# Kernel tuning notes

Hardware: AMD Instinct MI355X
Metric: run time of the kernel (lower is better)

Reference implementation:

```python
import jax, jax.numpy as jnp
import numpy as np

N_NODES = 50000
N_EDGES = 800000
IN_CH = 64
OUT_CH = 128
N_HEADS = 4
HEAD_DIM = OUT_CH // N_HEADS
LN_EPS = 1e-5


def setup_inputs() -> dict:
    key = jax.random.key(0)
    ks = jax.random.split(key, 12)
    def lin(k, fan_in, fan_out):
        bound = 1.0 / np.sqrt(fan_in)
        kw, kb = jax.random.split(k)
        W = jax.random.uniform(kw, (fan_in, fan_out), jnp.float32, -bound, bound)
        b = jax.random.uniform(kb, (fan_out,), jnp.float32, -bound, bound)
        return W, b
    Wq, bq = lin(ks[0], IN_CH, OUT_CH)
    Wk, bk = lin(ks[1], IN_CH, OUT_CH)
    Wv, bv = lin(ks[2], IN_CH, OUT_CH)
    We1, be1 = lin(ks[3], 2 * IN_CH, OUT_CH)
    We2, be2 = lin(ks[4], OUT_CH, N_HEADS)
    Wo, bo = lin(ks[5], OUT_CH, OUT_CH)
    gamma = jnp.ones((OUT_CH,), jnp.float32)
    beta = jnp.zeros((OUT_CH,), jnp.float32)
    x = jax.random.normal(ks[6], (N_NODES, IN_CH), jnp.float32)
    edge_index = jax.random.randint(ks[7], (2, N_EDGES), 0, N_NODES, jnp.int64 if jax.config.jax_enable_x64 else jnp.int32)
    return {"x": x, "edge_index": edge_index,
            "Wq": Wq, "bq": bq, "Wk": Wk, "bk": bk, "Wv": Wv, "bv": bv,
            "We1": We1, "be1": be1, "We2": We2, "be2": be2,
            "Wo": Wo, "bo": bo, "gamma": gamma, "beta": beta}


def reference(x, edge_index, Wq, bq, Wk, bk, Wv, bv, We1, be1, We2, be2, Wo, bo, gamma, beta):
    # Projections -> [N, H, Dh]
    q = (x @ Wq + bq).reshape(-1, N_HEADS, HEAD_DIM)
    k = (x @ Wk + bk).reshape(-1, N_HEADS, HEAD_DIM)
    v = (x @ Wv + bv).reshape(-1, N_HEADS, HEAD_DIM)
    src, dst = edge_index[0], edge_index[1]
    # Edge MLP attention weights: [E, H, 1]
    edge_features = jnp.concatenate([x[src], x[dst]], axis=-1)  # [E, 2*IN_CH]
    edge_weights = jax.nn.relu(edge_features @ We1 + be1) @ We2 + be2  # [E, H]
    edge_weights = edge_weights[:, :, None]
    # Attention logits per edge: [E, H, 1]
    attn = jnp.sum(q[dst] * k[src], axis=-1, keepdims=True)
    attn = attn * edge_weights / np.sqrt(HEAD_DIM).astype(np.float32)
    # Faithful to original: softmax over the edge dimension (dim=0)
    attn = jax.nn.softmax(attn, axis=0)
    # Weighted gather-scatter aggregation: [N, H, Dh]
    out = jax.ops.segment_sum(attn * v[src], dst, num_segments=N_NODES)
    out = out.reshape(-1, OUT_CH)
    # Output transform (dropout is identity in eval mode) + LayerNorm
    out = out @ Wo + bo
    mu = jnp.mean(out, axis=-1, keepdims=True)
    var = jnp.var(out, axis=-1, keepdims=True)
    out = (out - mu) * jax.lax.rsqrt(var + LN_EPS) * gamma + beta
    return out
```

## Files before the change

### kernel.cpp

```cpp
#include <hip/hip_runtime.h>
#include <hip/hip_bf16.h>

typedef __hip_bfloat16 bf16;
typedef __attribute__((ext_vector_type(8))) short short8;
typedef __attribute__((ext_vector_type(4))) float f32x4;
typedef __attribute__((ext_vector_type(2))) float f32x2;
typedef _Float16 h2 __attribute__((ext_vector_type(2)));

constexpr int NN = 50000;
constexpr int NE = 800000;
constexpr int IC = 64;
constexpr int OC = 128;
constexpr int NH = 4;
constexpr unsigned F32_ONE = 0x3F800000u;
constexpr float KC = 0.25503486f;

__device__ __forceinline__ float ldf(const void* p, int i, bool f32) {
    return f32 ? ((const float*)p)[i]
               : __bfloat162float(((const bf16*)p)[i]);
}

__device__ __forceinline__ int ld_idx(const void* p, long long i, bool i64) {
    return i64 ? (int)((const long long*)p)[i] : ((const int*)p)[i];
}

__device__ __forceinline__ bool probe_i64(const void* ei) {
    const unsigned* u = (const unsigned*)ei;
    return (u[1] | u[3] | u[5] | u[7]) == 0u;
}

__device__ __forceinline__ unsigned f2bu(float x) {
    unsigned u = __float_as_uint(x);
    return (u + 0x7FFFu + ((u >> 16) & 1u)) >> 16;
}

__device__ __forceinline__ h2 u2h(unsigned u) { return __builtin_bit_cast(h2, u); }

__device__ __forceinline__ float fdot2(h2 a, h2 b, float c) {
#if __has_builtin(__builtin_amdgcn_fdot2)
    return __builtin_amdgcn_fdot2(a, b, c, false);
#else
    return c + (float)a[0] * (float)b[0] + (float)a[1] * (float)b[1];
#endif
}

__device__ __forceinline__ h2 relu2(h2 a) {
    h2 z = {(_Float16)0.f, (_Float16)0.f};
#if __has_builtin(__builtin_elementwise_max)
    return __builtin_elementwise_max(a, z);
#else
    h2 r;
    r[0] = a[0] > (_Float16)0.f ? a[0] : (_Float16)0.f;
    r[1] = a[1] > (_Float16)0.f ? a[1] : (_Float16)0.f;
    return r;
#endif
}

#define DPPADD(x, ctrl) \
    ((x) + __int_as_float(__builtin_amdgcn_mov_dpp(__float_as_int(x), (ctrl), 0xF, 0xF, false)))

__device__ __forceinline__ int rfl(int v) { return __builtin_amdgcn_readfirstlane(v); }

__device__ __forceinline__ unsigned char f32_to_fp8(float x) {
#if __has_builtin(__builtin_amdgcn_cvt_pk_fp8_f32)
    return (unsigned char)(__builtin_amdgcn_cvt_pk_fp8_f32(x, x, 0, false) & 0xFF);
#else
    unsigned bits = __float_as_uint(x);
    unsigned s = bits >> 31;
    float a = fabsf(x);
    if (a >= 448.f) return (unsigned char)((s << 7) | 0x7E);
    if (a < 0.015625f) {
        int m = (int)(a * 512.f + 0.5f);
        if (m >= 8) return (unsigned char)((s << 7) | 0x08);
        return (unsigned char)((s << 7) | m);
    }
    unsigned ab = (bits & 0x7FFFFFFFu) + 0x00080000u;
    int e8 = (int)(ab >> 23) - 127 + 7;
    unsigned m3 = (ab >> 20) & 7u;
    if (e8 >= 16) return (unsigned char)((s << 7) | 0x7E);
    return (unsigned char)((s << 7) | ((unsigned)e8 << 3) | m3);
#endif
}

__device__ __forceinline__ void fp8x2_to_f32(unsigned u, float& f0, float& f1) {
#if __has_builtin(__builtin_amdgcn_cvt_pk_f32_fp8)
    f32x2 lo = __builtin_amdgcn_cvt_pk_f32_fp8(u, false);
    f0 = lo[0]; f1 = lo[1];
#else
    float r[2];
#pragma unroll
    for (int j = 0; j < 2; ++j) {
        unsigned b = (u >> (8 * j)) & 0xFF;
        unsigned s = b >> 7, e = (b >> 3) & 15, m = b & 7;
        float v = (e == 0) ? (float)m * 0.001953125f
                           : __uint_as_float(((e + 120u) << 23) | (m << 20));
        r[j] = s ? -v : v;
    }
    f0 = r[0]; f1 = r[1];
#endif
}

constexpr int PB_X   = 12500;
constexpr int PB_W   = 160;
constexpr int PB_WO  = 64;
constexpr int PB_CNT = 3125;

__global__ __launch_bounds__(256) void prep(
    const void* __restrict__ x,
    const void* __restrict__ Wq, const void* __restrict__ bq,
    const void* __restrict__ Wk, const void* __restrict__ bk,
    const void* __restrict__ Wv, const void* __restrict__ bv,
    const void* __restrict__ We1, const void* __restrict__ be1,
    const void* __restrict__ We2, const void* __restrict__ be2,
    const void* __restrict__ Wo,  const unsigned* __restrict__ gw,
    const void* __restrict__ eia, const void* __restrict__ eib, int split,
    bf16* __restrict__ xb, bf16* __restrict__ WcatT, bf16* __restrict__ WoT,
    int* __restrict__ cnt, int* __restrict__ rank,
    unsigned* __restrict__ We2h, float* __restrict__ be2f,
    float* __restrict__ bcat)
{
    const bool f32 = (gw[0] == F32_ONE);
    int b = blockIdx.x, t = threadIdx.x;
    if (b < PB_X) {
        int i = b * 256 + t;
        if (i < NN * IC) xb[i] = __float2bfloat16(ldf(x, i, f32));
    } else if (b < PB_X + PB_W) {
        int idx = (b - PB_X) * 256 + t;
        int n = idx >> 6, k = idx & 63;
        int sel = n >> 7, c = n & 127;
        float v;
        if (sel == 0)      v = ldf(Wq, k * OC + c, f32);
        else if (sel == 1) v = ldf(Wk, k * OC + c, f32);
        else if (sel == 2) v = ldf(Wv, k * OC + c, f32);
        else if (sel == 3) v = ldf(We1, k * OC + c, f32);
        else               v = ldf(We1, (IC + k) * OC + c, f32);
        WcatT[idx] = __float2bfloat16(v);
    } else if (b < PB_X + PB_W + PB_WO) {
        int idx = (b - PB_X - PB_W) * 256 + t;
        int n = idx >> 7, k = idx & 127;
        WoT[idx] = __float2bfloat16(ldf(Wo, k * OC + n, f32));
    } else if (b < PB_X + PB_W + PB_WO + PB_CNT) {
        const bool i64 = probe_i64(eia);
        long long e = (long long)(b - PB_X - PB_W - PB_WO) * 256 + t;
        int d = split ? ld_idx(eib, e, i64) : ld_idx(eia, NE + e, i64);
        int r = atomicAdd(&cnt[d], 1);
        rank[e] = r;
    } else {
        if (t < NH) be2f[t] = ldf(be2, t, f32);
        {
            int ln = t >> 2, k = t & 3;
            int g = ln >> 4, ii = ln & 15;
            int pp = 4 * ii + k;
            h2 hv;
            hv[0] = (_Float16)ldf(We2, (2 * pp) * NH + g, f32);
            hv[1] = (_Float16)ldf(We2, (2 * pp + 1) * NH + g, f32);
            We2h[t] = __builtin_bit_cast(unsigned, hv);
        }
        for (int n = t; n < 5 * OC; n += 256) {
            int sel = n >> 7, c = n & 127;
            float bb = 0.f;
            if (sel == 0) bb = ldf(bq, c, f32);
            else if (sel == 1) bb = ldf(bk, c, f32);
            else if (sel == 2) bb = ldf(bv, c, f32);
            else if (sel == 4) bb = ldf(be1, c, f32);
            bcat[n] = bb;
        }
    }
}

constexpr int SCAN_NB = 49;

__global__ __launch_bounds__(256) void scan_part(const int* __restrict__ cnt,
                                                 int* __restrict__ bsum,
                                                 int* __restrict__ rowptr)
{
    int b = blockIdx.x, t = threadIdx.x;
    int base = b * 1024 + t * 4;
    int4 v;
    if (base < NN) v = *(const int4*)(cnt + base);
    else { v.x = 0; v.y = 0; v.z = 0; v.w = 0; }
    int s = v.x + v.y + v.z + v.w;
#pragma unroll
    for (int off = 1; off < 64; off <<= 1) s += __shfl_xor(s, off);
    __shared__ int sm[4];
    int lane = t & 63, w = t >> 6;
    if (lane == 0) sm[w] = s;
    __syncthreads();
    if (t == 0) bsum[b] = sm[0] + sm[1] + sm[2] + sm[3];
    if (b == 0 && t == 0) rowptr[NN] = NE;
}

__global__ __launch_bounds__(256) void scan_fin(const int* __restrict__ cnt,
                                                const int* __restrict__ bsum,
                                                int* __restrict__ rowptr)
{
    int b = blockIdx.x, t = threadIdx.x;
    int lane = t & 63, w = t >> 6;
    __shared__ int s_boff;
    __shared__ int wsum[4];
    if (w == 0) {
        int pre = (lane < b) ? bsum[lane] : 0;
#pragma unroll
        for (int off = 1; off < 64; off <<= 1) pre += __shfl_xor(pre, off);
        if (lane == 0) s_boff = pre;
    }
    int base = b * 1024 + t * 4;
    int4 v;
    if (base < NN) v = *(const int4*)(cnt + base);
    else { v.x = 0; v.y = 0; v.z = 0; v.w = 0; }
    int s = v.x + v.y + v.z + v.w;
    int inc = s;
#pragma unroll
    for (int off = 1; off < 64; off <<= 1) {
        int u = __shfl_up(inc, off);
        if (lane >= off) inc += u;
    }
    if (lane == 63) wsum[w] = inc;
    __syncthreads();
    int run = s_boff + (inc - s);
#pragma unroll
    for (int i = 0; i < 3; ++i) if (i < w) run += wsum[i];
    if (base < NN) {
        int4 rp;
        rp.x = run;
        rp.y = rp.x + v.x;
        rp.z = rp.y + v.y;
        rp.w = rp.z + v.z;
        *(int4*)(rowptr + base) = rp;
    }
}

constexpr int NG_GEMM = 3125;
constexpr int NG_FILL = 3125;

__global__ __launch_bounds__(256) void node_gemm(
    const bf16* __restrict__ xb, const bf16* __restrict__ WcatT,
    const float* __restrict__ bcat,
    unsigned char* __restrict__ qb_dst, unsigned char* __restrict__ ka_src,
    unsigned char* __restrict__ vf8,
    const void* __restrict__ eia, const void* __restrict__ eib, int split,
    const int* __restrict__ rowptr, const int* __restrict__ rank,
    int* __restrict__ ssrc)
{
    if (blockIdx.x >= NG_GEMM) {
        const bool i64 = probe_i64(eia);
        long long e = (long long)(blockIdx.x - NG_GEMM) * 256 + threadIdx.x;
        int s = ld_idx(eia, e, i64);
        int d = split ? ld_idx(eib, e, i64) : ld_idx(eia, NE + e, i64);
        int pos = rowptr[d] + rank[e];
        ssrc[pos] = s;
        return;
    }
    int wave = threadIdx.x >> 6;
    int lane = threadIdx.x & 63;
    int quad = lane >> 4;
    int l16  = lane & 15;
    int row_base = blockIdx.x * 16;
    int m = row_base + l16;

    short8 a0 = *(const short8*)(xb + (size_t)m * IC + quad * 8);
    short8 a1 = *(const short8*)(xb + (size_t)m * IC + 32 + quad * 8);

    _Float16* qh = (_Float16*)qb_dst;
    _Float16* kh = (_Float16*)ka_src;

#pragma unroll
    for (int t = 0; t < 10; ++t) {
        int colbase = wave * 160 + t * 16;
        const bf16* bp = WcatT + (size_t)(colbase + l16) * IC + quad * 8;
        short8 b0 = *(const short8*)(bp);
        short8 b1 = *(const short8*)(bp + 32);
        f32x4 acc = {0.f, 0.f, 0.f, 0.f};
        acc = __builtin_amdgcn_mfma_f32_16x16x32_bf16(a0, b0, acc, 0, 0, 0);
        acc = __builtin_amdgcn_mfma_f32_16x16x32_bf16(a1, b1, acc, 0, 0, 0);

        float bias = bcat[colbase + l16];
        int sel = colbase >> 7;
        int cc  = (colbase & 127) + l16;
#pragma unroll
        for (int r = 0; r < 4; ++r) {
            int node = row_base + quad * 4 + r;
            float fv = acc[r] + bias;
            if (sel == 2) {
                vf8[(size_t)node * OC + cc] = f32_to_fp8(fv);
            } else {
                _Float16 val = (_Float16)fv;
                if (sel == 0)      qh[(size_t)node * 256 + cc] = val;
                else if (sel == 1) kh[(size_t)node * 256 + cc] = val;
                else if (sel == 3) kh[(size_t)node * 256 + 128 + cc] = val;
                else               qh[(size_t)node * 256 + 128 + cc] = val;
            }
        }
    }
}

__global__ __launch_bounds__(256) void edge_gather(
    const int* __restrict__ rowptr, const int* __restrict__ ssrc,
    unsigned char* __restrict__ qb_dst, const unsigned char* __restrict__ ka_src,
    const unsigned char* __restrict__ vf8,
    const unsigned* __restrict__ We2h, const float* __restrict__ be2f,
    float* __restrict__ spart)
{
    int node = rfl(blockIdx.x * 4 + (threadIdx.x >> 6));
    int lane = threadIdx.x & 63;
    int i16  = lane & 15;
    int myh  = lane >> 4;

    const unsigned char* drow = qb_dst + (size_t)node * 512;
    h2 dq = u2h(*(const unsigned*)(drow + lane * 4));
    uint4 dbu = *(const uint4*)(drow + 256 + 16 * i16);
    h2 db0 = u2h(dbu.x), db1 = u2h(dbu.y), db2 = u2h(dbu.z), db3 = u2h(dbu.w);

    uint4 wu = *(const uint4*)(We2h + lane * 4);
    h2 w0 = u2h(wu.x), w1 = u2h(wu.y), w2 = u2h(wu.z), w3 = u2h(wu.w);
    float be2h = be2f[myh];

    int beg = rfl(rowptr[node]);
    int end = rfl(rowptr[node + 1]);
    float o0 = 0.f, o1 = 0.f, s_acc = 0.f;

    if (beg < end) {
        int ib = (beg + 1 < end) ? beg + 1 : end - 1;
        int sa = rfl(ssrc[beg]);
        int sb = rfl(ssrc[ib]);
        const unsigned char* ra = ka_src + (size_t)sa * 512;
        const unsigned char* rb = ka_src + (size_t)sb * 512;
        unsigned kuA = *(const unsigned*)(ra + lane * 4);
        uint4    auA = *(const uint4*)(ra + 256 + 16 * i16);
        unsigned uvA = *(const unsigned short*)(vf8 + (size_t)sa * OC + 2 * lane);
        unsigned kuB = *(const unsigned*)(rb + lane * 4);
        uint4    auB = *(const uint4*)(rb + 256 + 16 * i16);
        unsigned uvB = *(const unsigned short*)(vf8 + (size_t)sb * OC + 2 * lane);
        int na = (beg + 2 < end) ? beg + 2 : end - 1;
        int nb = (beg + 3 < end) ? beg + 3 : end - 1;
        int sna = rfl(ssrc[na]);
        int snb = rfl(ssrc[nb]);

        for (int p = beg; p < end; p += 2) {
            const unsigned char* rc = ka_src + (size_t)sna * 512;
            const unsigned char* rd = ka_src + (size_t)snb * 512;
            unsigned kuC = *(const unsigned*)(rc + lane * 4);
            uint4    auC = *(const uint4*)(rc + 256 + 16 * i16);
            unsigned uvC = *(const unsigned short*)(vf8 + (size_t)sna * OC + 2 * lane);
            unsigned kuD = *(const unsigned*)(rd + lane * 4);
            uint4    auD = *(const uint4*)(rd + 256 + 16 * i16);
            unsigned uvD = *(const unsigned short*)(vf8 + (size_t)snb * OC + 2 * lane);
            int fa = (p + 4 < end) ? p + 4 : end - 1;
            int fb = (p + 5 < end) ? p + 5 : end - 1;
            int s4a = rfl(ssrc[fa]);
            int s4b = rfl(ssrc[fb]);

            bool hasB = (p + 1 < end);

            float tA = fdot2(u2h(kuA), dq, 0.f);
            float tB = fdot2(u2h(kuB), dq, 0.f);
            h2 hA0 = relu2(u2h(auA.x) + db0);
            h2 hA1 = relu2(u2h(auA.y) + db1);
            h2 hA2 = relu2(u2h(auA.z) + db2);
            h2 hA3 = relu2(u2h(auA.w) + db3);
            h2 hB0 = relu2(u2h(auB.x) + db0);
            h2 hB1 = relu2(u2h(auB.y) + db1);
            h2 hB2 = relu2(u2h(auB.z) + db2);
            h2 hB3 = relu2(u2h(auB.w) + db3);
            float pA = fdot2(hA3, w3, fdot2(hA2, w2, fdot2(hA1, w1, fdot2(hA0, w0, 0.f))));
            float pB = fdot2(hB3, w3, fdot2(hB2, w2, fdot2(hB1, w1, fdot2(hB0, w0, 0.f))));

            tA = DPPADD(tA, 0xB1);  pA = DPPADD(pA, 0xB1);
            tB = DPPADD(tB, 0xB1);  pB = DPPADD(pB, 0xB1);
            tA = DPPADD(tA, 0x4E);  pA = DPPADD(pA, 0x4E);
            tB = DPPADD(tB, 0x4E);  pB = DPPADD(pB, 0x4E);
            tA = DPPADD(tA, 0x128); pA = DPPADD(pA, 0x128);
            tB = DPPADD(tB, 0x128); pB = DPPADD(pB, 0x128);
            tA = DPPADD(tA, 0x124); pA = DPPADD(pA, 0x124);
            tB = DPPADD(tB, 0x124); pB = DPPADD(pB, 0x124);

            float coefA = exp2f(tA * (pA + be2h) * KC);
            float coefB = hasB ? exp2f(tB * (pB + be2h) * KC) : 0.f;
            s_acc += coefA + coefB;

            float vA0, vA1, vB0, vB1;
            fp8x2_to_f32(uvA, vA0, vA1);
            fp8x2_to_f32(uvB, vB0, vB1);
            o0 = fmaf(coefA, vA0, fmaf(coefB, vB0, o0));
            o1 = fmaf(coefA, vA1, fmaf(coefB, vB1, o1));

            kuA = kuC; auA = auC; uvA = uvC;
            kuB = kuD; auB = auD; uvB = uvD;
            sna = s4a; snb = s4b;
        }
    }
    *(unsigned*)(qb_dst + (size_t)node * 512 + lane * 4) = f2bu(o0) | (f2bu(o1) << 16);
    if (i16 == 0) spart[node * 4 + myh] = s_acc;
}

constexpr int SR_BLOCKS = 98;
__global__ __launch_bounds__(256) void s_reduce(const float* __restrict__ spart,
                                                float* __restrict__ ssum)
{
    int tid = blockIdx.x * 256 + threadIdx.x;
    int h = threadIdx.x & 3;
    float s = 0.f;
    for (int i = tid; i < NN * 4; i += SR_BLOCKS * 256) s += spart[i];
#pragma unroll
    for (int off = 4; off <= 32; off <<= 1) s += __shfl_xor(s, off);
    __shared__ float sm[4][4];
    int lane = threadIdx.x & 63, w = threadIdx.x >> 6;
    if (lane < 4) sm[w][h] = s;
    __syncthreads();
    if (threadIdx.x < 4) {
        float tot = sm[0][h] + sm[1][h] + sm[2][h] + sm[3][h];
        atomicAdd(&ssum[h], tot);
    }
}

__global__ __launch_bounds__(256) void out_gemm(
    const unsigned char* __restrict__ aggv, const bf16* __restrict__ WoT,
    const void* __restrict__ bo, const void* __restrict__ gamma,
    const void* __restrict__ beta, const unsigned* __restrict__ gw,
    const float* __restrict__ ssum,
    void* __restrict__ out)
{
    const bool f32 = (gw[0] == F32_ONE);
    int wave = threadIdx.x >> 6;
    int lane = threadIdx.x & 63;
    int quad = lane >> 4;
    int l16  = lane & 15;
    int rb = blockIdx.x * 64 + wave * 16;
    int m = rb + l16;
    int ma = (m < NN) ? m : 0;

    const bf16* arow = (const bf16*)(aggv + (size_t)ma * 512);
    short8 a[4];
#pragma unroll
    for (int h = 0; h < 4; ++h) {
        short8 raw = *(const short8*)(arow + h * 32 + quad * 8);
        float invh = 1.0f / ssum[h];
#pragma unroll
        for (int jj = 0; jj < 8; ++jj) {
            float f = __uint_as_float(((unsigned)(unsigned short)raw[jj]) << 16) * invh;
            raw[jj] = (short)f2bu(f);
        }
        a[h] = raw;
    }

    float o[8][4];
#pragma unroll
    for (int t = 0; t < 8; ++t) {
        const bf16* bp = WoT + (size_t)(t * 16 + l16) * OC + quad * 8;
        f32x4 acc = {0.f, 0.f, 0.f, 0.f};
#pragma unroll
        for (int h = 0; h < 4; ++h) {
            short8 bfr = *(const short8*)(bp + h * 32);
            acc = __builtin_amdgcn_mfma_f32_16x16x32_bf16(a[h], bfr, acc, 0, 0, 0);
        }
        float bias = ldf(bo, t * 16 + l16, f32);
#pragma unroll
        for (int r = 0; r < 4; ++r) o[t][r] = acc[r] + bias;
    }

#pragma unroll
    for (int r = 0; r < 4; ++r) {
        float s1 = 0.f, s2 = 0.f;
#pragma unroll
        for (int t = 0; t < 8; ++t) { s1 += o[t][r]; s2 += o[t][r] * o[t][r]; }
#pragma unroll
        for (int off = 1; off <= 8; off <<= 1) {
            s1 += __shfl_xor(s1, off);
            s2 += __shfl_xor(s2, off);
        }
        float mu = s1 * (1.0f / OC);
        float var = fmaxf(s2 * (1.0f / OC) - mu * mu, 0.f);
        float rs = rsqrtf(var + 1e-5f);
        int node = rb + quad * 4 + r;
        if (node < NN) {
#pragma unroll
            for (int t = 0; t < 8; ++t) {
                int col = t * 16 + l16;
                float y = (o[t][r] - mu) * rs * ldf(gamma, col, f32) + ldf(beta, col, f32);
                if (f32) ((float*)out)[(size_t)node * OC + col] = y;
                else     ((bf16*)out)[(size_t)node * OC + col] = __float2bfloat16(y);
            }
        }
    }
}

extern "C" void kernel_launch(void* const* d_in, const int* in_sizes, int n_in,
                              void* d_out, int out_size, void* d_ws, size_t ws_size,
                              hipStream_t stream)
{
    int p = 0;
    const void* x   = d_in[p++];
    const void* eia = d_in[p++];
    const void* eib = eia;
    int split = 0;
    if (n_in >= 17) { eib = d_in[p++]; split = 1; }
    const void* Wq   = d_in[p++];
    const void* bq   = d_in[p++];
    const void* Wk   = d_in[p++];
    const void* bk   = d_in[p++];
    const void* Wv   = d_in[p++];
    const void* bv   = d_in[p++];
    const void* We1  = d_in[p++];
    const void* be1  = d_in[p++];
    const void* We2  = d_in[p++];
    const void* be2  = d_in[p++];
    const void* Wo   = d_in[p++];
    const void* bo   = d_in[p++];
    const void* gamma= d_in[p++];
    const void* beta = d_in[p++];
    const unsigned* gw = (const unsigned*)gamma;

    char* w = (char*)d_ws;
    bf16*  xb     = (bf16*)w;                  w += (size_t)NN * IC * 2;
    unsigned char* qb_dst = (unsigned char*)w; w += (size_t)NN * 512;
    unsigned char* ka_src = (unsigned char*)w; w += (size_t)NN * 512;
    unsigned char* vf8    = (unsigned char*)w; w += (size_t)NN * OC;
    int*   ssrc   = (int*)w;                   w += (size_t)NE * 4;
    int*   rank   = (int*)w;                   w += (size_t)NE * 4;
    int*   cnt    = (int*)w;                   w += (size_t)NN * 4;
    float* ssum   = (float*)w;                 w += 8 * 4;
    int*   rowptr = (int*)w;                   w += (size_t)(NN + 4) * 4;
    int*   bsum   = (int*)w;                   w += 64 * 4;
    float* spart  = (float*)w;                 w += (size_t)NN * 4 * 4;
    unsigned* We2h = (unsigned*)w;             w += 256 * 4;
    float* be2f   = (float*)w;                 w += NH * 4;
    bf16*  WcatT  = (bf16*)w;                  w += (size_t)5 * OC * IC * 2;
    float* bcat   = (float*)w;                 w += 5 * OC * 4;
    bf16*  WoT    = (bf16*)w;                  w += (size_t)OC * OC * 2;

    if (ws_size < (size_t)((char*)w - (char*)d_ws)) return;

    hipMemsetAsync(cnt, 0, (size_t)NN * 4 + 32, stream);
    prep<<<PB_X + PB_W + PB_WO + PB_CNT + 1, 256, 0, stream>>>(
        x, Wq, bq, Wk, bk, Wv, bv, We1, be1, We2, be2, Wo, gw,
        eia, eib, split,
        xb, WcatT, WoT, cnt, rank, We2h, be2f, bcat);
    scan_part<<<SCAN_NB, 256, 0, stream>>>(cnt, bsum, rowptr);
    scan_fin<<<SCAN_NB, 256, 0, stream>>>(cnt, bsum, rowptr);
    node_gemm<<<NG_GEMM + NG_FILL, 256, 0, stream>>>(
        xb, WcatT, bcat, qb_dst, ka_src, vf8, eia, eib, split, rowptr, rank, ssrc);
    edge_gather<<<NN / 4, 256, 0, stream>>>(rowptr, ssrc, qb_dst, ka_src, vf8,
                                            We2h, be2f, spart);
    s_reduce<<<SR_BLOCKS, 256, 0, stream>>>(spart, ssum);
    out_gemm<<<(NN + 63) / 64, 256, 0, stream>>>(qb_dst, WoT, bo, gamma, beta, gw,
                                                 ssum, d_out);
}
```

Measured before the change: 291.9 us.

## Compute edge logits and edge MLP with MFMA over 16-edge tiles

Restructures the per-node edge gather so 16 incoming edges are processed at once. Each lane loads a slice of a source row, and MFMA 16x16x32 f16 instructions compute the q·k dot products and the projection of the hidden edge MLP onto the four heads. This replaces the per-edge fdot2 chains and DPP reductions. The 16 coefficients are then broadcast through ds_bpermute for the fp8 value accumulation, which runs as a serial 16-step loop with a scalar readlane per edge. The change drops the previous two-edge software prefetch, and nodes with few edges (about 16 on average) may waste lanes in partial tiles.

```diff
diff --git a/kernel.cpp b/kernel.cpp
--- a/kernel.cpp
+++ b/kernel.cpp
@@ -6,6 +6,7 @@
 typedef __attribute__((ext_vector_type(4))) float f32x4;
 typedef __attribute__((ext_vector_type(2))) float f32x2;
 typedef _Float16 h2 __attribute__((ext_vector_type(2)));
+typedef _Float16 h8 __attribute__((ext_vector_type(8)));
 
 constexpr int NN = 50000;
 constexpr int NE = 800000;
@@ -35,29 +36,6 @@
 }
 
 __device__ __forceinline__ h2 u2h(unsigned u) { return __builtin_bit_cast(h2, u); }
-
-__device__ __forceinline__ float fdot2(h2 a, h2 b, float c) {
-#if __has_builtin(__builtin_amdgcn_fdot2)
-    return __builtin_amdgcn_fdot2(a, b, c, false);
-#else
-    return c + (float)a[0] * (float)b[0] + (float)a[1] * (float)b[1];
-#endif
-}
-
-__device__ __forceinline__ h2 relu2(h2 a) {
-    h2 z = {(_Float16)0.f, (_Float16)0.f};
-#if __has_builtin(__builtin_elementwise_max)
-    return __builtin_elementwise_max(a, z);
-#else
-    h2 r;
-    r[0] = a[0] > (_Float16)0.f ? a[0] : (_Float16)0.f;
-    r[1] = a[1] > (_Float16)0.f ? a[1] : (_Float16)0.f;
-    return r;
-#endif
-}
-
-#define DPPADD(x, ctrl) \
-    ((x) + __int_as_float(__builtin_amdgcn_mov_dpp(__float_as_int(x), (ctrl), 0xF, 0xF, false)))
 
 __device__ __forceinline__ int rfl(int v) { return __builtin_amdgcn_readfirstlane(v); }
 
@@ -116,7 +94,7 @@
     const void* __restrict__ eia, const void* __restrict__ eib, int split,
     bf16* __restrict__ xb, bf16* __restrict__ WcatT, bf16* __restrict__ WoT,
     int* __restrict__ cnt, int* __restrict__ rank,
-    unsigned* __restrict__ We2h, float* __restrict__ be2f,
+    _Float16* __restrict__ We2f, float* __restrict__ be2f,
     float* __restrict__ bcat)
 {
     const bool f32 = (gw[0] == F32_ONE);
@@ -148,13 +126,14 @@
     } else {
         if (t < NH) be2f[t] = ldf(be2, t, f32);
         {
-            int ln = t >> 2, k = t & 3;
-            int g = ln >> 4, ii = ln & 15;
-            int pp = 4 * ii + k;
-            h2 hv;
-            hv[0] = (_Float16)ldf(We2, (2 * pp) * NH + g, f32);
-            hv[1] = (_Float16)ldf(We2, (2 * pp + 1) * NH + g, f32);
-            We2h[t] = __builtin_bit_cast(unsigned, hv);
+            int kb = t >> 6, ln = t & 63;
+            int g = ln & 15, qd = ln >> 4;
+            _Float16* dst = We2f + (size_t)t * 8;
+#pragma unroll
+            for (int j = 0; j < 8; ++j) {
+                float v = (g < 4) ? ldf(We2, (32 * kb + qd * 8 + j) * NH + g, f32) : 0.f;
+                dst[j] = (_Float16)v;
+            }
         }
         for (int n = t; n < 5 * OC; n += 256) {
             int sel = n >> 7, c = n & 127;
@@ -298,99 +277,102 @@
     const int* __restrict__ rowptr, const int* __restrict__ ssrc,
     unsigned char* __restrict__ qb_dst, const unsigned char* __restrict__ ka_src,
     const unsigned char* __restrict__ vf8,
-    const unsigned* __restrict__ We2h, const float* __restrict__ be2f,
+    const _Float16* __restrict__ We2f, const float* __restrict__ be2f,
     float* __restrict__ spart)
 {
     int node = rfl(blockIdx.x * 4 + (threadIdx.x >> 6));
     int lane = threadIdx.x & 63;
-    int i16  = lane & 15;
-    int myh  = lane >> 4;
-
-    const unsigned char* drow = qb_dst + (size_t)node * 512;
-    h2 dq = u2h(*(const unsigned*)(drow + lane * 4));
-    uint4 dbu = *(const uint4*)(drow + 256 + 16 * i16);
-    h2 db0 = u2h(dbu.x), db1 = u2h(dbu.y), db2 = u2h(dbu.z), db3 = u2h(dbu.w);
-
-    uint4 wu = *(const uint4*)(We2h + lane * 4);
-    h2 w0 = u2h(wu.x), w1 = u2h(wu.y), w2 = u2h(wu.z), w3 = u2h(wu.w);
-    float be2h = be2f[myh];
+    int l16  = lane & 15;
+    int quad = lane >> 4;
+
+    const _Float16* drow = (const _Float16*)(qb_dst + (size_t)node * 512);
+    h8 hz = {};
+    h8 bq[4], bp_[4], bw[4];
+#pragma unroll
+    for (int kb = 0; kb < 4; ++kb) {
+        h8 qv  = *(const h8*)(drow + kb * 32 + quad * 8);
+        bp_[kb] = *(const h8*)(drow + 128 + kb * 32 + quad * 8);
+        bq[kb] = (l16 == kb) ? qv : hz;
+        bw[kb] = *(const h8*)(We2f + (size_t)((kb << 6) + lane) * 8);
+    }
+    float be2h = be2f[l16 & 3];
 
     int beg = rfl(rowptr[node]);
     int end = rfl(rowptr[node + 1]);
-    float o0 = 0.f, o1 = 0.f, s_acc = 0.f;
-
-    if (beg < end) {
-        int ib = (beg + 1 < end) ? beg + 1 : end - 1;
-        int sa = rfl(ssrc[beg]);
-        int sb = rfl(ssrc[ib]);
-        const unsigned char* ra = ka_src + (size_t)sa * 512;
-        const unsigned char* rb = ka_src + (size_t)sb * 512;
-        unsigned kuA = *(const unsigned*)(ra + lane * 4);
-        uint4    auA = *(const uint4*)(ra + 256 + 16 * i16);
-        unsigned uvA = *(const unsigned short*)(vf8 + (size_t)sa * OC + 2 * lane);
-        unsigned kuB = *(const unsigned*)(rb + lane * 4);
-        uint4    auB = *(const uint4*)(rb + 256 + 16 * i16);
-        unsigned uvB = *(const unsigned short*)(vf8 + (size_t)sb * OC + 2 * lane);
-        int na = (beg + 2 < end) ? beg + 2 : end - 1;
-        int nb = (beg + 3 < end) ? beg + 3 : end - 1;
-        int sna = rfl(ssrc[na]);
-        int snb = rfl(ssrc[nb]);
-
-        for (int p = beg; p < end; p += 2) {
-            const unsigned char* rc = ka_src + (size_t)sna * 512;
-            const unsigned char* rd = ka_src + (size_t)snb * 512;
-            unsigned kuC = *(const unsigned*)(rc + lane * 4);
-            uint4    auC = *(const uint4*)(rc + 256 + 16 * i16);
-            unsigned uvC = *(const unsigned short*)(vf8 + (size_t)sna * OC + 2 * lane);
-            unsigned kuD = *(const unsigned*)(rd + lane * 4);
-            uint4    auD = *(const uint4*)(rd + 256 + 16 * i16);
-            unsigned uvD = *(const unsigned short*)(vf8 + (size_t)snb * OC + 2 * lane);
-            int fa = (p + 4 < end) ? p + 4 : end - 1;
-            int fb = (p + 5 < end) ? p + 5 : end - 1;
-            int s4a = rfl(ssrc[fa]);
-            int s4b = rfl(ssrc[fb]);
-
-            bool hasB = (p + 1 < end);
-
-            float tA = fdot2(u2h(kuA), dq, 0.f);
-            float tB = fdot2(u2h(kuB), dq, 0.f);
-            h2 hA0 = relu2(u2h(auA.x) + db0);
-            h2 hA1 = relu2(u2h(auA.y) + db1);
-            h2 hA2 = relu2(u2h(auA.z) + db2);
-            h2 hA3 = relu2(u2h(auA.w) + db3);
-            h2 hB0 = relu2(u2h(auB.x) + db0);
-            h2 hB1 = relu2(u2h(auB.y) + db1);
-            h2 hB2 = relu2(u2h(auB.z) + db2);
-            h2 hB3 = relu2(u2h(auB.w) + db3);
-            float pA = fdot2(hA3, w3, fdot2(hA2, w2, fdot2(hA1, w1, fdot2(hA0, w0, 0.f))));
-            float pB = fdot2(hB3, w3, fdot2(hB2, w2, fdot2(hB1, w1, fdot2(hB0, w0, 0.f))));
-
-            tA = DPPADD(tA, 0xB1);  pA = DPPADD(pA, 0xB1);
-            tB = DPPADD(tB, 0xB1);  pB = DPPADD(pB, 0xB1);
-            tA = DPPADD(tA, 0x4E);  pA = DPPADD(pA, 0x4E);
-            tB = DPPADD(tB, 0x4E);  pB = DPPADD(pB, 0x4E);
-            tA = DPPADD(tA, 0x128); pA = DPPADD(pA, 0x128);
-            tB = DPPADD(tB, 0x128); pB = DPPADD(pB, 0x128);
-            tA = DPPADD(tA, 0x124); pA = DPPADD(pA, 0x124);
-            tB = DPPADD(tB, 0x124); pB = DPPADD(pB, 0x124);
-
-            float coefA = exp2f(tA * (pA + be2h) * KC);
-            float coefB = hasB ? exp2f(tB * (pB + be2h) * KC) : 0.f;
-            s_acc += coefA + coefB;
-
-            float vA0, vA1, vB0, vB1;
-            fp8x2_to_f32(uvA, vA0, vA1);
-            fp8x2_to_f32(uvB, vB0, vB1);
-            o0 = fmaf(coefA, vA0, fmaf(coefB, vB0, o0));
-            o1 = fmaf(coefA, vA1, fmaf(coefB, vB1, o1));
-
-            kuA = kuC; auA = auC; uvA = uvC;
-            kuB = kuD; auB = auD; uvB = uvD;
-            sna = s4a; snb = s4b;
-        }
-    }
+    float o0 = 0.f, o1 = 0.f, s_lane = 0.f;
+    int vh4 = quad * 4;
+
+    for (int t0 = beg; t0 < end; t0 += 16) {
+        int idx = t0 + l16;
+        idx = (idx < end) ? idx : end - 1;
+        int sv = ssrc[idx];
+        const _Float16* arow = (const _Float16*)(ka_src + (size_t)sv * 512);
+
+        h8 ak0 = *(const h8*)(arow + 0  + quad * 8);
+        h8 ak1 = *(const h8*)(arow + 32 + quad * 8);
+        h8 ak2 = *(const h8*)(arow + 64 + quad * 8);
+        h8 ak3 = *(const h8*)(arow + 96 + quad * 8);
+        h8 aa0 = *(const h8*)(arow + 128 + 0  + quad * 8);
+        h8 aa1 = *(const h8*)(arow + 128 + 32 + quad * 8);
+        h8 aa2 = *(const h8*)(arow + 128 + 64 + quad * 8);
+        h8 aa3 = *(const h8*)(arow + 128 + 96 + quad * 8);
+
+        f32x4 at = {0.f, 0.f, 0.f, 0.f};
+        f32x4 ap = {0.f, 0.f, 0.f, 0.f};
+        at = __builtin_amdgcn_mfma_f32_16x16x32_f16(ak0, bq[0], at, 0, 0, 0);
+        at = __builtin_amdgcn_mfma_f32_16x16x32_f16(ak1, bq[1], at, 0, 0, 0);
+        at = __builtin_amdgcn_mfma_f32_16x16x32_f16(ak2, bq[2], at, 0, 0, 0);
+        at = __builtin_amdgcn_mfma_f32_16x16x32_f16(ak3, bq[3], at, 0, 0, 0);
+
+#if __has_builtin(__builtin_elementwise_max)
+        h8 h0 = __builtin_elementwise_max(aa0 + bp_[0], hz);
+        h8 h1 = __builtin_elementwise_max(aa1 + bp_[1], hz);
+        h8 h2v = __builtin_elementwise_max(aa2 + bp_[2], hz);
+        h8 h3 = __builtin_elementwise_max(aa3 + bp_[3], hz);
+#else
+        h8 h0 = aa0 + bp_[0], h1 = aa1 + bp_[1], h2v = aa2 + bp_[2], h3 = aa3 + bp_[3];
+#pragma unroll
+        for (int j = 0; j < 8; ++j) {
+            h0[j] = h0[j] > (_Float16)0.f ? h0[j] : (_Float16)0.f;
+            h1[j] = h1[j] > (_Float16)0.f ? h1[j] : (_Float16)0.f;
+            h2v[j] = h2v[j] > (_Float16)0.f ? h2v[j] : (_Float16)0.f;
+            h3[j] = h3[j] > (_Float16)0.f ? h3[j] : (_Float16)0.f;
+        }
+#endif
+        ap = __builtin_amdgcn_mfma_f32_16x16x32_f16(h0, bw[0], ap, 0, 0, 0);
+        ap = __builtin_amdgcn_mfma_f32_16x16x32_f16(h1, bw[1], ap, 0, 0, 0);
+        ap = __builtin_amdgcn_mfma_f32_16x16x32_f16(h2v, bw[2], ap, 0, 0, 0);
+        ap = __builtin_amdgcn_mfma_f32_16x16x32_f16(h3, bw[3], ap, 0, 0, 0);
+
+        float coef[4];
+#pragma unroll
+        for (int r = 0; r < 4; ++r) {
+            bool valid = (t0 + quad * 4 + r) < end;
+            float c = exp2f(at[r] * (ap[r] + be2h) * KC);
+            c = valid ? c : 0.f;
+            coef[r] = c;
+            s_lane += c;
+        }
+
+#pragma unroll
+        for (int e = 0; e < 16; ++e) {
+            if (t0 + e < end) {
+                int se = __builtin_amdgcn_readlane(sv, e);
+                unsigned uv = *(const unsigned short*)(vf8 + (size_t)se * OC + 2 * lane);
+                float cf = __int_as_float(__builtin_amdgcn_ds_bpermute(
+                    vh4 + 64 * (e >> 2), __float_as_int(coef[e & 3])));
+                float v0, v1;
+                fp8x2_to_f32(uv, v0, v1);
+                o0 = fmaf(cf, v0, o0);
+                o1 = fmaf(cf, v1, o1);
+            }
+        }
+    }
+
     *(unsigned*)(qb_dst + (size_t)node * 512 + lane * 4) = f2bu(o0) | (f2bu(o1) << 16);
-    if (i16 == 0) spart[node * 4 + myh] = s_acc;
+    float s1 = s_lane + __shfl_xor(s_lane, 16);
+    float s2 = s1 + __shfl_xor(s1, 32);
+    if (lane < 4) spart[node * 4 + lane] = s2;
 }
 
 constexpr int SR_BLOCKS = 98;
@@ -522,7 +504,7 @@
     int*   rowptr = (int*)w;                   w += (size_t)(NN + 4) * 4;
     int*   bsum   = (int*)w;                   w += 64 * 4;
     float* spart  = (float*)w;                 w += (size_t)NN * 4 * 4;
-    unsigned* We2h = (unsigned*)w;             w += 256 * 4;
+    _Float16* We2f = (_Float16*)w;             w += 2048 * 2;
     float* be2f   = (float*)w;                 w += NH * 4;
     bf16*  WcatT  = (bf16*)w;                  w += (size_t)5 * OC * IC * 2;
     float* bcat   = (float*)w;                 w += 5 * OC * 4;
@@ -534,13 +516,13 @@
     prep<<<PB_X + PB_W + PB_WO + PB_CNT + 1, 256, 0, stream>>>(
         x, Wq, bq, Wk, bk, Wv, bv, We1, be1, We2, be2, Wo, gw,
         eia, eib, split,
-        xb, WcatT, WoT, cnt, rank, We2h, be2f, bcat);
+        xb, WcatT, WoT, cnt, rank, We2f, be2f, bcat);
     scan_part<<<SCAN_NB, 256, 0, stream>>>(cnt, bsum, rowptr);
     scan_fin<<<SCAN_NB, 256, 0, stream>>>(cnt, bsum, rowptr);
     node_gemm<<<NG_GEMM + NG_FILL, 256, 0, stream>>>(
         xb, WcatT, bcat, qb_dst, ka_src, vf8, eia, eib, split, rowptr, rank, ssrc);
     edge_gather<<<NN / 4, 256, 0, stream>>>(rowptr, ssrc, qb_dst, ka_src, vf8,
-                                            We2h, be2f, spart);
+                                            We2f, be2f, spart);
     s_reduce<<<SR_BLOCKS, 256, 0, stream>>>(spart, ssum);
     out_gemm<<<(NN + 63) / 64, 256, 0, stream>>>(qb_dst, WoT, bo, gamma, beta, gw,
                                                  ssum, d_out);
```

Result: slower. 364.1 us (+24.7%).

## Process eight edges per wave in parallel in edge_gather with 8-lane sub-groups

Applied to the files above, without the earlier changes.

Restructures the edge_gather loop so each wave splits into 8 slots of 8 lanes, and each slot computes one edge's attention logit and edge-MLP score over 32-byte chunks. The old loop handled two edges per iteration across all 64 lanes. We2 is re-laid-out so each lane holds weights for all four heads, and the reduction is shortened to DPP plus a swizzle. The per-edge coefficients are then broadcast with ds_bpermute for the value accumulation. This aims to cut the serial per-edge dependency chain and the cross-lane reduction cost, at the price of more registers, a bpermute per edge, and wasted slots when a node has few edges.

```diff
diff --git a/kernel.cpp b/kernel.cpp
--- a/kernel.cpp
+++ b/kernel.cpp
@@ -58,6 +58,8 @@
 
 #define DPPADD(x, ctrl) \
     ((x) + __int_as_float(__builtin_amdgcn_mov_dpp(__float_as_int(x), (ctrl), 0xF, 0xF, false)))
+#define SWZADD4(x) \
+    ((x) + __int_as_float(__builtin_amdgcn_ds_swizzle(__float_as_int(x), 0x101F)))
 
 __device__ __forceinline__ int rfl(int v) { return __builtin_amdgcn_readfirstlane(v); }
 
@@ -148,12 +150,10 @@
     } else {
         if (t < NH) be2f[t] = ldf(be2, t, f32);
         {
-            int ln = t >> 2, k = t & 3;
-            int g = ln >> 4, ii = ln & 15;
-            int pp = 4 * ii + k;
+            int sub = t >> 5, g = (t >> 3) & 3, j = t & 7;
             h2 hv;
-            hv[0] = (_Float16)ldf(We2, (2 * pp) * NH + g, f32);
-            hv[1] = (_Float16)ldf(We2, (2 * pp + 1) * NH + g, f32);
+            hv[0] = (_Float16)ldf(We2, (16 * sub + 2 * j) * NH + g, f32);
+            hv[1] = (_Float16)ldf(We2, (16 * sub + 2 * j + 1) * NH + g, f32);
             We2h[t] = __builtin_bit_cast(unsigned, hv);
         }
         for (int n = t; n < 5 * OC; n += 256) {
@@ -303,94 +303,122 @@
 {
     int node = rfl(blockIdx.x * 4 + (threadIdx.x >> 6));
     int lane = threadIdx.x & 63;
-    int i16  = lane & 15;
+    int slot = lane >> 3;
+    int sub  = lane & 7;
     int myh  = lane >> 4;
 
     const unsigned char* drow = qb_dst + (size_t)node * 512;
-    h2 dq = u2h(*(const unsigned*)(drow + lane * 4));
-    uint4 dbu = *(const uint4*)(drow + 256 + 16 * i16);
-    h2 db0 = u2h(dbu.x), db1 = u2h(dbu.y), db2 = u2h(dbu.z), db3 = u2h(dbu.w);
-
-    uint4 wu = *(const uint4*)(We2h + lane * 4);
-    h2 w0 = u2h(wu.x), w1 = u2h(wu.y), w2 = u2h(wu.z), w3 = u2h(wu.w);
-    float be2h = be2f[myh];
+    uint4 dq0 = *(const uint4*)(drow + 32 * sub);
+    uint4 dq1 = *(const uint4*)(drow + 32 * sub + 16);
+    uint4 db0 = *(const uint4*)(drow + 256 + 32 * sub);
+    uint4 db1 = *(const uint4*)(drow + 256 + 32 * sub + 16);
+
+    const unsigned* wp = We2h + sub * 32;
+    uint4 w0a = *(const uint4*)(wp +  0), w0b = *(const uint4*)(wp +  4);
+    uint4 w1a = *(const uint4*)(wp +  8), w1b = *(const uint4*)(wp + 12);
+    uint4 w2a = *(const uint4*)(wp + 16), w2b = *(const uint4*)(wp + 20);
+    uint4 w3a = *(const uint4*)(wp + 24), w3b = *(const uint4*)(wp + 28);
+    float be2l = be2f[sub >> 1];
+    const bool sb2 = (sub & 2) != 0;
+    const bool sb4 = (sub & 4) != 0;
 
     int beg = rfl(rowptr[node]);
     int end = rfl(rowptr[node + 1]);
-    float o0 = 0.f, o1 = 0.f, s_acc = 0.f;
+    float o0 = 0.f, o1 = 0.f, s_loc = 0.f;
 
     if (beg < end) {
-        int ib = (beg + 1 < end) ? beg + 1 : end - 1;
-        int sa = rfl(ssrc[beg]);
-        int sb = rfl(ssrc[ib]);
-        const unsigned char* ra = ka_src + (size_t)sa * 512;
-        const unsigned char* rb = ka_src + (size_t)sb * 512;
-        unsigned kuA = *(const unsigned*)(ra + lane * 4);
-        uint4    auA = *(const uint4*)(ra + 256 + 16 * i16);
-        unsigned uvA = *(const unsigned short*)(vf8 + (size_t)sa * OC + 2 * lane);
-        unsigned kuB = *(const unsigned*)(rb + lane * 4);
-        uint4    auB = *(const uint4*)(rb + 256 + 16 * i16);
-        unsigned uvB = *(const unsigned short*)(vf8 + (size_t)sb * OC + 2 * lane);
-        int na = (beg + 2 < end) ? beg + 2 : end - 1;
-        int nb = (beg + 3 < end) ? beg + 3 : end - 1;
-        int sna = rfl(ssrc[na]);
-        int snb = rfl(ssrc[nb]);
-
-        for (int p = beg; p < end; p += 2) {
-            const unsigned char* rc = ka_src + (size_t)sna * 512;
-            const unsigned char* rd = ka_src + (size_t)snb * 512;
-            unsigned kuC = *(const unsigned*)(rc + lane * 4);
-            uint4    auC = *(const uint4*)(rc + 256 + 16 * i16);
-            unsigned uvC = *(const unsigned short*)(vf8 + (size_t)sna * OC + 2 * lane);
-            unsigned kuD = *(const unsigned*)(rd + lane * 4);
-            uint4    auD = *(const uint4*)(rd + 256 + 16 * i16);
-            unsigned uvD = *(const unsigned short*)(vf8 + (size_t)snb * OC + 2 * lane);
-            int fa = (p + 4 < end) ? p + 4 : end - 1;
-            int fb = (p + 5 < end) ? p + 5 : end - 1;
-            int s4a = rfl(ssrc[fa]);
-            int s4b = rfl(ssrc[fb]);
-
-            bool hasB = (p + 1 < end);
-
-            float tA = fdot2(u2h(kuA), dq, 0.f);
-            float tB = fdot2(u2h(kuB), dq, 0.f);
-            h2 hA0 = relu2(u2h(auA.x) + db0);
-            h2 hA1 = relu2(u2h(auA.y) + db1);
-            h2 hA2 = relu2(u2h(auA.z) + db2);
-            h2 hA3 = relu2(u2h(auA.w) + db3);
-            h2 hB0 = relu2(u2h(auB.x) + db0);
-            h2 hB1 = relu2(u2h(auB.y) + db1);
-            h2 hB2 = relu2(u2h(auB.z) + db2);
-            h2 hB3 = relu2(u2h(auB.w) + db3);
-            float pA = fdot2(hA3, w3, fdot2(hA2, w2, fdot2(hA1, w1, fdot2(hA0, w0, 0.f))));
-            float pB = fdot2(hB3, w3, fdot2(hB2, w2, fdot2(hB1, w1, fdot2(hB0, w0, 0.f))));
-
-            tA = DPPADD(tA, 0xB1);  pA = DPPADD(pA, 0xB1);
-            tB = DPPADD(tB, 0xB1);  pB = DPPADD(pB, 0xB1);
-            tA = DPPADD(tA, 0x4E);  pA = DPPADD(pA, 0x4E);
-            tB = DPPADD(tB, 0x4E);  pB = DPPADD(pB, 0x4E);
-            tA = DPPADD(tA, 0x128); pA = DPPADD(pA, 0x128);
-            tB = DPPADD(tB, 0x128); pB = DPPADD(pB, 0x128);
-            tA = DPPADD(tA, 0x124); pA = DPPADD(pA, 0x124);
-            tB = DPPADD(tB, 0x124); pB = DPPADD(pB, 0x124);
-
-            float coefA = exp2f(tA * (pA + be2h) * KC);
-            float coefB = hasB ? exp2f(tB * (pB + be2h) * KC) : 0.f;
-            s_acc += coefA + coefB;
-
-            float vA0, vA1, vB0, vB1;
-            fp8x2_to_f32(uvA, vA0, vA1);
-            fp8x2_to_f32(uvB, vB0, vB1);
-            o0 = fmaf(coefA, vA0, fmaf(coefB, vB0, o0));
-            o1 = fmaf(coefA, vA1, fmaf(coefB, vB1, o1));
-
-            kuA = kuC; auA = auC; uvA = uvC;
-            kuB = kuD; auB = auD; uvB = uvD;
-            sna = s4a; snb = s4b;
+        int endm1 = end - 1;
+        int idx = beg + slot; idx = (idx < end) ? idx : endm1;
+        int sv = ssrc[idx];
+        const unsigned char* r = ka_src + (size_t)sv * 512 + 32 * sub;
+        uint4 k0 = *(const uint4*)(r);
+        uint4 k1 = *(const uint4*)(r + 16);
+        uint4 a0 = *(const uint4*)(r + 256);
+        uint4 a1 = *(const uint4*)(r + 272);
+
+        for (int t0 = beg; t0 < end; t0 += 8) {
+            int idxn = t0 + 8 + slot; idxn = (idxn < end) ? idxn : endm1;
+            int svn = ssrc[idxn];
+            const unsigned char* rn = ka_src + (size_t)svn * 512 + 32 * sub;
+            uint4 kn0 = *(const uint4*)(rn);
+            uint4 kn1 = *(const uint4*)(rn + 16);
+            uint4 an0 = *(const uint4*)(rn + 256);
+            uint4 an1 = *(const uint4*)(rn + 272);
+
+            float tt = fdot2(u2h(k0.x), u2h(dq0.x), 0.f);
+            tt = fdot2(u2h(k0.y), u2h(dq0.y), tt);
+            tt = fdot2(u2h(k0.z), u2h(dq0.z), tt);
+            tt = fdot2(u2h(k0.w), u2h(dq0.w), tt);
+            tt = fdot2(u2h(k1.x), u2h(dq1.x), tt);
+            tt = fdot2(u2h(k1.y), u2h(dq1.y), tt);
+            tt = fdot2(u2h(k1.z), u2h(dq1.z), tt);
+            tt = fdot2(u2h(k1.w), u2h(dq1.w), tt);
+
+            h2 hh0 = relu2(u2h(a0.x) + u2h(db0.x));
+            h2 hh1 = relu2(u2h(a0.y) + u2h(db0.y));
+            h2 hh2 = relu2(u2h(a0.z) + u2h(db0.z));
+            h2 hh3 = relu2(u2h(a0.w) + u2h(db0.w));
+            h2 hh4 = relu2(u2h(a1.x) + u2h(db1.x));
+            h2 hh5 = relu2(u2h(a1.y) + u2h(db1.y));
+            h2 hh6 = relu2(u2h(a1.z) + u2h(db1.z));
+            h2 hh7 = relu2(u2h(a1.w) + u2h(db1.w));
+
+            float p0 = fdot2(hh0, u2h(w0a.x), 0.f);
+            float p1 = fdot2(hh0, u2h(w1a.x), 0.f);
+            float p2 = fdot2(hh0, u2h(w2a.x), 0.f);
+            float p3 = fdot2(hh0, u2h(w3a.x), 0.f);
+            p0 = fdot2(hh1, u2h(w0a.y), p0); p1 = fdot2(hh1, u2h(w1a.y), p1);
+            p2 = fdot2(hh1, u2h(w2a.y), p2); p3 = fdot2(hh1, u2h(w3a.y), p3);
+            p0 = fdot2(hh2, u2h(w0a.z), p0); p1 = fdot2(hh2, u2h(w1a.z), p1);
+            p2 = fdot2(hh2, u2h(w2a.z), p2); p3 = fdot2(hh2, u2h(w3a.z), p3);
+            p0 = fdot2(hh3, u2h(w0a.w), p0); p1 = fdot2(hh3, u2h(w1a.w), p1);
+            p2 = fdot2(hh3, u2h(w2a.w), p2); p3 = fdot2(hh3, u2h(w3a.w), p3);
+            p0 = fdot2(hh4, u2h(w0b.x), p0); p1 = fdot2(hh4, u2h(w1b.x), p1);
+            p2 = fdot2(hh4, u2h(w2b.x), p2); p3 = fdot2(hh4, u2h(w3b.x), p3);
+            p0 = fdot2(hh5, u2h(w0b.y), p0); p1 = fdot2(hh5, u2h(w1b.y), p1);
+            p2 = fdot2(hh5, u2h(w2b.y), p2); p3 = fdot2(hh5, u2h(w3b.y), p3);
+            p0 = fdot2(hh6, u2h(w0b.z), p0); p1 = fdot2(hh6, u2h(w1b.z), p1);
+            p2 = fdot2(hh6, u2h(w2b.z), p2); p3 = fdot2(hh6, u2h(w3b.z), p3);
+            p0 = fdot2(hh7, u2h(w0b.w), p0); p1 = fdot2(hh7, u2h(w1b.w), p1);
+            p2 = fdot2(hh7, u2h(w2b.w), p2); p3 = fdot2(hh7, u2h(w3b.w), p3);
+
+            tt = DPPADD(tt, 0xB1);
+            p0 = DPPADD(p0, 0xB1); p1 = DPPADD(p1, 0xB1);
+            p2 = DPPADD(p2, 0xB1); p3 = DPPADD(p3, 0xB1);
+            p0 = DPPADD(p0, 0x4E); p1 = DPPADD(p1, 0x4E);
+            p2 = DPPADD(p2, 0x4E); p3 = DPPADD(p3, 0x4E);
+            p0 = SWZADD4(p0); p1 = SWZADD4(p1);
+            p2 = SWZADD4(p2); p3 = SWZADD4(p3);
+
+            float pa = sb2 ? p1 : p0;
+            float pb = sb2 ? p3 : p2;
+            float ps = sb4 ? pb : pa;
+            float c = exp2f(tt * (ps + be2l) * KC);
+            c = (t0 + slot < end) ? c : 0.f;
+            s_loc += c;
+
+#pragma unroll
+            for (int e = 0; e < 8; ++e) {
+                if (t0 + e < end) {
+                    int se = __builtin_amdgcn_readlane(sv, 8 * e);
+                    unsigned uv = *(const unsigned short*)(vf8 + (size_t)se * OC + 2 * lane);
+                    float cf = __int_as_float(__builtin_amdgcn_ds_bpermute(
+                        4 * (8 * e + 2 * myh), __float_as_int(c)));
+                    float v0, v1;
+                    fp8x2_to_f32(uv, v0, v1);
+                    o0 = fmaf(cf, v0, o0);
+                    o1 = fmaf(cf, v1, o1);
+                }
+            }
+
+            k0 = kn0; k1 = kn1; a0 = an0; a1 = an1; sv = svn;
         }
     }
     *(unsigned*)(qb_dst + (size_t)node * 512 + lane * 4) = f2bu(o0) | (f2bu(o1) << 16);
-    if (i16 == 0) spart[node * 4 + myh] = s_acc;
+    s_loc += __shfl_xor(s_loc, 8);
+    s_loc += __shfl_xor(s_loc, 16);
+    s_loc += __shfl_xor(s_loc, 32);
+    if (slot == 0 && (sub & 1) == 0) spart[node * 4 + (sub >> 1)] = s_loc;
 }
 
 constexpr int SR_BLOCKS = 98;
```

Measured after the change: 355.8 us. +21.9%, slower.
